# Optimization experiments

Hardware: AMD Instinct MI355X
Metric: run time of the kernel (lower is better)

## Reference

```python
import jax, jax.numpy as jnp
import numpy as np

K = 16          # neighbors (min(k, N) with N=1024 -> 16)
HID = 64        # hidden_dim
NFEAT = 64      # num_features
LN_EPS = 1e-5


def _block(h, W, b, g, beta, a):
    # Linear -> LayerNorm -> PReLU (single shared slope a, torch default)
    h = jnp.einsum('...i,oi->...o', h, W) + b
    mu = jnp.mean(h, axis=-1, keepdims=True)
    var = jnp.mean((h - mu) ** 2, axis=-1, keepdims=True)
    h = g * (h - mu) / jnp.sqrt(var + LN_EPS) + beta
    return jnp.where(h > 0, h, a * h)


def setup_inputs() -> dict:
    key = jax.random.key(0)
    ks = jax.random.split(key, 12)
    B, N, D, F, H = 16, 1024, 3, NFEAT, HID
    points = jax.random.normal(ks[0], (B, N, D), dtype=jnp.float32)
    x = jax.random.normal(ks[1], (B, N, F), dtype=jnp.float32)
    mask = jax.random.randint(ks[2], (B, N), 0, 2, dtype=jnp.int32)
    s0 = 1.0 / np.sqrt(2 * F)
    sh = 1.0 / np.sqrt(H)
    W0 = jax.random.uniform(ks[3], (H, 2 * F), jnp.float32, -s0, s0)
    b0 = jax.random.uniform(ks[4], (H,), jnp.float32, -s0, s0)
    Wh = jax.random.uniform(ks[5], (4, H, H), jnp.float32, -sh, sh)  # 3 hidden + 1 final
    bh = jax.random.uniform(ks[6], (4, H), jnp.float32, -sh, sh)
    ln_g = jnp.ones((5, H), dtype=jnp.float32)
    ln_b = jnp.zeros((5, H), dtype=jnp.float32)
    prelu_a = jnp.full((5,), 0.25, dtype=jnp.float32)
    return {"points": points, "x": x, "mask": mask, "W0": W0, "b0": b0,
            "Wh": Wh, "bh": bh, "ln_g": ln_g, "ln_b": ln_b, "prelu_a": prelu_a}


def reference(points, x, mask, W0, b0, Wh, bh, ln_g, ln_b, prelu_a):
    B, N, _ = points.shape
    F = x.shape[-1]
    # pairwise euclidean distances, invalid columns -> +inf
    delta = points[:, :, None, :] - points[:, None, :, :]          # [B,N,N,D]
    dist = jnp.sqrt(jnp.sum(delta * delta, axis=-1))               # [B,N,N]
    dist = jnp.where(mask.astype(bool)[:, None, :], dist, jnp.inf)
    # k smallest distances -> neighbor indices
    _, idx = jax.lax.top_k(-dist, K)                               # [B,N,K]
    n_tracks = jnp.sum(mask.astype(jnp.float32), axis=-1)          # [B]
    neighbors = x[jnp.arange(B)[:, None, None], idx]               # [B,N,K,F]
    xc = jnp.broadcast_to(x[:, :, None, :], (B, N, K, F))
    h = jnp.concatenate([xc, x[:, :, None, :] - neighbors], axis=-1)  # [B,N,K,2F]
    h = _block(h, W0, b0, ln_g[0], ln_b[0], prelu_a[0])
    for i in range(4):
        h = _block(h, Wh[i], bh[i], ln_g[i + 1], ln_b[i + 1], prelu_a[i + 1])
    # masked mean over neighbor slots (mask uses original n_tracks)
    nm = (jnp.arange(K)[None, None, :] < n_tracks[:, None, None]).astype(jnp.float32)  # [B,N,K]
    n_safe = jnp.where(n_tracks == 0, 1.0, n_tracks)
    aggregated = jnp.sum(h * nm[..., None], axis=-2) / n_safe[:, None, None]
    return aggregated
```

## Files before the change

### kernel.cpp

```cpp
#include <hip/hip_runtime.h>
#include <hip/hip_bf16.h>
#include <math.h>

#define N_ 1024
#define KNN_K 16
#define LN_EPS 1e-5f

typedef unsigned long long u64;
typedef unsigned int u32;
typedef __attribute__((ext_vector_type(4))) float f32x4;
typedef __attribute__((ext_vector_type(8))) short short8;
typedef __attribute__((ext_vector_type(2))) unsigned int u32x2;
typedef __attribute__((ext_vector_type(4))) unsigned int u32x4;

__device__ __forceinline__ u32 rn_hi32(float v) {
  u32 u = __float_as_uint(v);
  return (u + 0x7FFFu + ((u >> 16) & 1u)) & 0xFFFF0000u;
}
__device__ __forceinline__ u32 rn_b16(float v) {
  u32 u = __float_as_uint(v);
  return (u + 0x7FFFu + ((u >> 16) & 1u)) >> 16;
}

__global__ __launch_bounds__(256) void front_kernel(
    const float* __restrict__ Wh, u32x4* __restrict__ whi,
    u32x4* __restrict__ wlo, const int* __restrict__ mask,
    float* __restrict__ ntr, const float* __restrict__ points,
    int* __restrict__ knn, const float* __restrict__ x,
    const float* __restrict__ W0, const float* __restrict__ b0,
    float* __restrict__ p_c, float* __restrict__ p_n) {
  __shared__ float SM[8192];
  const int blk = blockIdx.x;
  const int t = threadIdx.x;

  if (blk < 8) {
    int idx = blk * 256 + t;
    int lane = idx & 63;
    int ks = (idx >> 6) & 1;
    int m = (idx >> 7) & 3;
    int li = idx >> 9;
    int o = 16 * m + (lane & 15);
    int k0 = 32 * ks + 8 * (lane >> 4);
    const float* w = Wh + li * 4096 + o * 64 + k0;
    u32x4 hi, lo;
#pragma unroll
    for (int j = 0; j < 4; j++) {
      float f0 = w[2 * j], f1 = w[2 * j + 1];
      u32 h0 = rn_hi32(f0);
      u32 h1 = rn_hi32(f1);
      float l0 = f0 - __uint_as_float(h0);
      float l1 = f1 - __uint_as_float(h1);
      hi[j] = (h0 >> 16) | h1;
      lo[j] = rn_b16(l0) | (rn_b16(l1) << 16);
    }
    int fi = ((li * 4 + m) * 2 + ks) * 64 + lane;
    whi[fi] = hi;
    wlo[fi] = lo;
  } else if (blk < 24) {
    int b = blk - 8;
    int s = 0;
    for (int e = t; e < N_; e += 256) s += mask[b * N_ + e];
    for (int off = 32; off; off >>= 1) s += __shfl_xor(s, off, 64);
    int* accI = (int*)SM;
    int wave = t >> 6, lane = t & 63;
    if (lane == 0) accI[wave] = s;
    __syncthreads();
    if (t == 0) ntr[b] = (float)(accI[0] + accI[1] + accI[2] + accI[3]);
  } else if (blk < 24 + 4096) {
#pragma clang fp contract(off)
    float* px = SM;
    float* py = SM + 1024;
    float* pz = SM + 2048;
    float* minf = SM + 3072;
    int kb = blk - 24;
    int b = kb >> 8;
    int qbase = (kb & 255) << 2;
    for (int j = t; j < N_; j += 256) {
      const float* p = points + ((size_t)(b * N_ + j)) * 3;
      px[j] = p[0];
      py[j] = p[1];
      pz[j] = p[2];
      minf[j] = mask[b * N_ + j] ? 0.0f : __builtin_inff();
    }
    __syncthreads();
    int wave = t >> 6, lane = t & 63;
    int n = qbase + wave;
    float qx = px[n], qy = py[n], qz = pz[n];
    u64 key[16];
#pragma unroll
    for (int c = 0; c < 16; c++) {
      int j = lane + (c << 6);
      float dx = qx - px[j];
      float dy = qy - py[j];
      float dz = qz - pz[j];
      float d2 = dx * dx + dy * dy + dz * dz;
      d2 = d2 + minf[j];
      key[c] = ((u64)__float_as_uint(d2) << 32) | (u32)j;
    }
    int* dst = knn + ((size_t)(b * N_ + n)) * KNN_K;
    for (int s = 0; s < 16; s++) {
      u64 m = key[0];
#pragma unroll
      for (int c = 1; c < 16; c++) m = key[c] < m ? key[c] : m;
#pragma unroll
      for (int off = 32; off; off >>= 1) {
        u64 o = __shfl_xor(m, off, 64);
        if (o < m) m = o;
      }
      if (lane == 0) dst[s] = (int)(m & 0xFFFFFFFFu);
#pragma unroll
      for (int c = 0; c < 16; c++)
        if (key[c] == m) key[c] = ~0ULL;
    }
  } else {
    float* Wc = SM;
    float* Wn = SM + 4096;
    int pb = blk - (24 + 4096);
    for (int e = t; e < 4096; e += 256) {
      int o = e & 63, i = e >> 6;
      float wa = W0[o * 128 + i];
      float wb = W0[o * 128 + 64 + i];
      Wc[i * 64 + o] = wa + wb;
      Wn[i * 64 + o] = wb;
    }
    __syncthreads();
    int wave = t >> 6, lane = t & 63;
    int pbase = pb * 64 + wave * 16;
    for (int it = 0; it < 16; it++) {
      int p = pbase + it;
      const float* xr = x + (size_t)__builtin_amdgcn_readfirstlane(p) * 64;
      float pc = b0[lane];
      float pn = 0.0f;
#pragma unroll
      for (int i = 0; i < 64; i++) {
        float xi = xr[i];
        pc = fmaf(xi, Wc[i * 64 + lane], pc);
        pn = fmaf(xi, Wn[i * 64 + lane], pn);
      }
      p_c[(size_t)p * 64 + lane] = pc;
      p_n[(size_t)p * 64 + lane] = pn;
    }
  }
}

__global__ __launch_bounds__(128) void layerA_kernel(
    const float* __restrict__ p_c, const float* __restrict__ p_n,
    const int* __restrict__ knn_, const u32x4* __restrict__ whi,
    const u32x4* __restrict__ wlo, const float* __restrict__ bh,
    const float* __restrict__ ln_g, const float* __restrict__ ln_b,
    const float* __restrict__ prelu_a, u32* __restrict__ Hout) {
  const int t = threadIdx.x;
  const int wv = t >> 6, l = t & 63;
  const int c = l & 15;
  const int g = l >> 4;
  const int pbase = blockIdx.x * 8 + wv * 4;
  const int b = pbase >> 10;

  u32x4 bhi[4][2], blo[4][2];

  {
    float h[64];
    int p0 = pbase + g;
    int j = knn_[(size_t)p0 * 16 + c];
    const float4* pc4 = reinterpret_cast<const float4*>(p_c + (size_t)p0 * 64);
    const float4* pn4 = reinterpret_cast<const float4*>(p_n + (size_t)((b << 10) + j) * 64);
#pragma unroll
    for (int q = 0; q < 16; q++) {
      float4 a = pc4[q], v = pn4[q];
      h[q * 4 + 0] = a.x - v.x;
      h[q * 4 + 1] = a.y - v.y;
      h[q * 4 + 2] = a.z - v.z;
      h[q * 4 + 3] = a.w - v.w;
    }
    float s = 0.0f, s2 = 0.0f;
#pragma unroll
    for (int o = 0; o < 64; o++) { s += h[o]; s2 += h[o] * h[o]; }
    float mu = s * (1.0f / 64.0f);
    float var = s2 * (1.0f / 64.0f) - mu * mu;
    float inv = rsqrtf(var + LN_EPS);
    float aslope = prelu_a[0];
#pragma unroll
    for (int o = 0; o < 64; o++) {
      float v = ln_g[o] * ((h[o] - mu) * inv) + ln_b[o];
      h[o] = v > 0.0f ? v : aslope * v;
    }
    u32 hpk_hi[32], hpk_lo[32];
#pragma unroll
    for (int w = 0; w < 32; w++) {
      float f0 = h[2 * w], f1 = h[2 * w + 1];
      u32 h0 = rn_hi32(f0);
      u32 h1 = rn_hi32(f1);
      float l0 = f0 - __uint_as_float(h0);
      float l1 = f1 - __uint_as_float(h1);
      hpk_hi[w] = (h0 >> 16) | h1;
      hpk_lo[w] = rn_b16(l0) | (rn_b16(l1) << 16);
    }
#pragma unroll
    for (int nt = 0; nt < 4; nt++) {
      int src = c + 16 * nt;
#pragma unroll
      for (int ks = 0; ks < 2; ks++)
#pragma unroll
        for (int gw = 0; gw < 4; gw++)
#pragma unroll
          for (int j2 = 0; j2 < 4; j2++) {
            u32 th = (u32)__shfl((int)hpk_hi[16 * ks + 4 * gw + j2], src, 64);
            u32 tl = (u32)__shfl((int)hpk_lo[16 * ks + 4 * gw + j2], src, 64);
            if (g == gw) {
              bhi[nt][ks][j2] = th;
              blo[nt][ks][j2] = tl;
            }
          }
    }
  }

  const int li = 0;
  f32x4 bias4[4];
#pragma unroll
  for (int m = 0; m < 4; m++)
    bias4[m] = *(const f32x4*)(bh + li * 64 + 16 * m + 4 * g);

  f32x4 acc[4][4];
#pragma unroll
  for (int m = 0; m < 4; m++)
#pragma unroll
    for (int nt = 0; nt < 4; nt++) acc[m][nt] = bias4[m];

#pragma unroll
  for (int ks = 0; ks < 2; ks++)
#pragma unroll
    for (int m = 0; m < 4; m++) {
      int fi = ((li * 4 + m) * 2 + ks) * 64 + l;
      short8 ah = __builtin_bit_cast(short8, whi[fi]);
      short8 al = __builtin_bit_cast(short8, wlo[fi]);
#pragma unroll
      for (int nt = 0; nt < 4; nt++) {
        short8 bh_ = __builtin_bit_cast(short8, bhi[nt][ks]);
        short8 bl_ = __builtin_bit_cast(short8, blo[nt][ks]);
        acc[m][nt] = __builtin_amdgcn_mfma_f32_16x16x32_bf16(ah, bh_, acc[m][nt], 0, 0, 0);
        acc[m][nt] = __builtin_amdgcn_mfma_f32_16x16x32_bf16(ah, bl_, acc[m][nt], 0, 0, 0);
        acc[m][nt] = __builtin_amdgcn_mfma_f32_16x16x32_bf16(al, bh_, acc[m][nt], 0, 0, 0);
      }
    }

  f32x4 g4[4], b4[4];
#pragma unroll
  for (int m = 0; m < 4; m++) {
    g4[m] = *(const f32x4*)(ln_g + (li + 1) * 64 + 16 * m + 4 * g);
    b4[m] = *(const f32x4*)(ln_b + (li + 1) * 64 + 16 * m + 4 * g);
  }
  float aslope = prelu_a[li + 1];
#pragma unroll
  for (int nt = 0; nt < 4; nt++) {
    float s = 0.0f, s2 = 0.0f;
#pragma unroll
    for (int m = 0; m < 4; m++)
#pragma unroll
      for (int v = 0; v < 4; v++) {
        float x = acc[m][nt][v];
        s += x;
        s2 = fmaf(x, x, s2);
      }
    s += __shfl_xor(s, 16, 64);
    s2 += __shfl_xor(s2, 16, 64);
    s += __shfl_xor(s, 32, 64);
    s2 += __shfl_xor(s2, 32, 64);
    float mu = s * (1.0f / 64.0f);
    float var = s2 * (1.0f / 64.0f) - mu * mu;
    float inv = rsqrtf(var + LN_EPS);
#pragma unroll
    for (int m = 0; m < 4; m++)
#pragma unroll
      for (int v = 0; v < 4; v++) {
        float x = (acc[m][nt][v] - mu) * inv;
        x = g4[m][v] * x + b4[m][v];
        acc[m][nt][v] = x > 0.0f ? x : aslope * x;
      }
  }

#pragma unroll
  for (int nt = 0; nt < 4; nt++) {
    size_t eb = ((size_t)(pbase + nt) * 16 + c) * 32;
#pragma unroll
    for (int m = 0; m < 4; m++) {
      u32x2 v;
      v[0] = rn_b16(acc[m][nt][0]) | (rn_b16(acc[m][nt][1]) << 16);
      v[1] = rn_b16(acc[m][nt][2]) | (rn_b16(acc[m][nt][3]) << 16);
      *(u32x2*)(Hout + eb + 8 * m + 2 * g) = v;
    }
  }
}

__global__ __launch_bounds__(128) void layer_kernel(
    const u32* __restrict__ Hin, u32* __restrict__ Hout,
    const u32x4* __restrict__ whi, const u32x4* __restrict__ wlo,
    const float* __restrict__ bh, const float* __restrict__ ln_g,
    const float* __restrict__ ln_b, const float* __restrict__ prelu_a,
    const float* __restrict__ ntr, float* __restrict__ out, int li, int last) {
  const int t = threadIdx.x;
  const int wv = t >> 6, l = t & 63;
  const int c = l & 15;
  const int g = l >> 4;
  const int pbase = blockIdx.x * 8 + wv * 4;
  const int b = pbase >> 10;

  u32x4 bw[4][2];
#pragma unroll
  for (int nt = 0; nt < 4; nt++) {
    size_t eb = ((size_t)(pbase + nt) * 16 + c) * 32;
#pragma unroll
    for (int ks = 0; ks < 2; ks++)
      bw[nt][ks] = *(const u32x4*)(Hin + eb + 16 * ks + 4 * g);
  }

  f32x4 bias4[4];
#pragma unroll
  for (int m = 0; m < 4; m++)
    bias4[m] = *(const f32x4*)(bh + li * 64 + 16 * m + 4 * g);

  f32x4 acc[4][4];
#pragma unroll
  for (int m = 0; m < 4; m++)
#pragma unroll
    for (int nt = 0; nt < 4; nt++) acc[m][nt] = bias4[m];

#pragma unroll
  for (int ks = 0; ks < 2; ks++)
#pragma unroll
    for (int m = 0; m < 4; m++) {
      int fi = ((li * 4 + m) * 2 + ks) * 64 + l;
      short8 ah = __builtin_bit_cast(short8, whi[fi]);
      short8 al = __builtin_bit_cast(short8, wlo[fi]);
#pragma unroll
      for (int nt = 0; nt < 4; nt++) {
        short8 bb = __builtin_bit_cast(short8, bw[nt][ks]);
        acc[m][nt] = __builtin_amdgcn_mfma_f32_16x16x32_bf16(ah, bb, acc[m][nt], 0, 0, 0);
        acc[m][nt] = __builtin_amdgcn_mfma_f32_16x16x32_bf16(al, bb, acc[m][nt], 0, 0, 0);
      }
    }

  f32x4 g4[4], b4[4];
#pragma unroll
  for (int m = 0; m < 4; m++) {
    g4[m] = *(const f32x4*)(ln_g + (li + 1) * 64 + 16 * m + 4 * g);
    b4[m] = *(const f32x4*)(ln_b + (li + 1) * 64 + 16 * m + 4 * g);
  }
  float aslope = prelu_a[li + 1];
#pragma unroll
  for (int nt = 0; nt < 4; nt++) {
    float s = 0.0f, s2 = 0.0f;
#pragma unroll
    for (int m = 0; m < 4; m++)
#pragma unroll
      for (int v = 0; v < 4; v++) {
        float x = acc[m][nt][v];
        s += x;
        s2 = fmaf(x, x, s2);
      }
    s += __shfl_xor(s, 16, 64);
    s2 += __shfl_xor(s2, 16, 64);
    s += __shfl_xor(s, 32, 64);
    s2 += __shfl_xor(s2, 32, 64);
    float mu = s * (1.0f / 64.0f);
    float var = s2 * (1.0f / 64.0f) - mu * mu;
    float inv = rsqrtf(var + LN_EPS);
#pragma unroll
    for (int m = 0; m < 4; m++)
#pragma unroll
      for (int v = 0; v < 4; v++) {
        float x = (acc[m][nt][v] - mu) * inv;
        x = g4[m][v] * x + b4[m][v];
        acc[m][nt][v] = x > 0.0f ? x : aslope * x;
      }
  }

  if (!last) {
#pragma unroll
    for (int nt = 0; nt < 4; nt++) {
      size_t eb = ((size_t)(pbase + nt) * 16 + c) * 32;
#pragma unroll
      for (int m = 0; m < 4; m++) {
        u32x2 v;
        v[0] = rn_b16(acc[m][nt][0]) | (rn_b16(acc[m][nt][1]) << 16);
        v[1] = rn_b16(acc[m][nt][2]) | (rn_b16(acc[m][nt][3]) << 16);
        *(u32x2*)(Hout + eb + 8 * m + 2 * g) = v;
      }
    }
  } else {
    float cnt = ntr[b];
    float n_safe = (cnt == 0.0f) ? 1.0f : cnt;
    float rinv = 1.0f / n_safe;
    float msk = ((float)c < cnt) ? 1.0f : 0.0f;
#pragma unroll
    for (int nt = 0; nt < 4; nt++)
#pragma unroll
      for (int m = 0; m < 4; m++) {
        f32x4 r;
#pragma unroll
        for (int v = 0; v < 4; v++) {
          float x = acc[m][nt][v] * msk;
          x += __shfl_xor(x, 1, 64);
          x += __shfl_xor(x, 2, 64);
          x += __shfl_xor(x, 4, 64);
          x += __shfl_xor(x, 8, 64);
          r[v] = x * rinv;
        }
        if (c == 0)
          *(f32x4*)(out + (size_t)(pbase + nt) * 64 + 16 * m + 4 * g) = r;
      }
  }
}

__global__ __launch_bounds__(128) void mlp_mfma3_kernel(
    const float* __restrict__ p_c, const float* __restrict__ p_n,
    const int* __restrict__ knn_, const u32x4* __restrict__ whi,
    const u32x4* __restrict__ wlo, const float* __restrict__ bh,
    const float* __restrict__ ln_g, const float* __restrict__ ln_b,
    const float* __restrict__ prelu_a, const float* __restrict__ ntr,
    float* __restrict__ out) {
  const int t = threadIdx.x;
  const int wv = t >> 6, l = t & 63;
  const int c = l & 15;
  const int g = l >> 4;
  const int pbase = blockIdx.x * 8 + wv * 4;
  const int b = pbase >> 10;

  u32x4 bhi[4][2], blo[4][2];

  {
    float h[64];
    int p0 = pbase + g;
    int j = knn_[(size_t)p0 * 16 + c];
    const float4* pc4 = reinterpret_cast<const float4*>(p_c + (size_t)p0 * 64);
    const float4* pn4 = reinterpret_cast<const float4*>(p_n + (size_t)((b << 10) + j) * 64);
#pragma unroll
    for (int q = 0; q < 16; q++) {
      float4 a = pc4[q], v = pn4[q];
      h[q * 4 + 0] = a.x - v.x;
      h[q * 4 + 1] = a.y - v.y;
      h[q * 4 + 2] = a.z - v.z;
      h[q * 4 + 3] = a.w - v.w;
    }
    float s = 0.0f, s2 = 0.0f;
#pragma unroll
    for (int o = 0; o < 64; o++) { s += h[o]; s2 += h[o] * h[o]; }
    float mu = s * (1.0f / 64.0f);
    float var = s2 * (1.0f / 64.0f) - mu * mu;
    float inv = rsqrtf(var + LN_EPS);
    float aslope = prelu_a[0];
#pragma unroll
    for (int o = 0; o < 64; o++) {
      float v = ln_g[o] * ((h[o] - mu) * inv) + ln_b[o];
      h[o] = v > 0.0f ? v : aslope * v;
    }
    u32 hpk_hi[32], hpk_lo[32];
#pragma unroll
    for (int w = 0; w < 32; w++) {
      float f0 = h[2 * w], f1 = h[2 * w + 1];
      u32 h0 = rn_hi32(f0);
      u32 h1 = rn_hi32(f1);
      float l0 = f0 - __uint_as_float(h0);
      float l1 = f1 - __uint_as_float(h1);
      hpk_hi[w] = (h0 >> 16) | h1;
      hpk_lo[w] = rn_b16(l0) | (rn_b16(l1) << 16);
    }
#pragma unroll
    for (int nt = 0; nt < 4; nt++) {
      int src = c + 16 * nt;
#pragma unroll
      for (int ks = 0; ks < 2; ks++)
#pragma unroll
        for (int gw = 0; gw < 4; gw++)
#pragma unroll
          for (int j2 = 0; j2 < 4; j2++) {
            u32 th = (u32)__shfl((int)hpk_hi[16 * ks + 4 * gw + j2], src, 64);
            u32 tl = (u32)__shfl((int)hpk_lo[16 * ks + 4 * gw + j2], src, 64);
            if (g == gw) {
              bhi[nt][ks][j2] = th;
              blo[nt][ks][j2] = tl;
            }
          }
    }
  }

  float cnt = ntr[b];

#pragma unroll 1
  for (int li = 0; li < 4; li++) {
    f32x4 bias4[4];
#pragma unroll
    for (int m = 0; m < 4; m++)
      bias4[m] = *(const f32x4*)(bh + li * 64 + 16 * m + 4 * g);

    f32x4 acc[4][4];
#pragma unroll
    for (int m = 0; m < 4; m++)
#pragma unroll
      for (int nt = 0; nt < 4; nt++) acc[m][nt] = bias4[m];

#pragma unroll
    for (int ks = 0; ks < 2; ks++)
#pragma unroll
      for (int m = 0; m < 4; m++) {
        int fi = ((li * 4 + m) * 2 + ks) * 64 + l;
        short8 ah = __builtin_bit_cast(short8, whi[fi]);
        short8 al = __builtin_bit_cast(short8, wlo[fi]);
#pragma unroll
        for (int nt = 0; nt < 4; nt++) {
          short8 bh_ = __builtin_bit_cast(short8, bhi[nt][ks]);
          short8 bl_ = __builtin_bit_cast(short8, blo[nt][ks]);
          acc[m][nt] = __builtin_amdgcn_mfma_f32_16x16x32_bf16(ah, bh_, acc[m][nt], 0, 0, 0);
          acc[m][nt] = __builtin_amdgcn_mfma_f32_16x16x32_bf16(ah, bl_, acc[m][nt], 0, 0, 0);
          acc[m][nt] = __builtin_amdgcn_mfma_f32_16x16x32_bf16(al, bh_, acc[m][nt], 0, 0, 0);
        }
      }

    f32x4 g4[4], b4[4];
#pragma unroll
    for (int m = 0; m < 4; m++) {
      g4[m] = *(const f32x4*)(ln_g + (li + 1) * 64 + 16 * m + 4 * g);
      b4[m] = *(const f32x4*)(ln_b + (li + 1) * 64 + 16 * m + 4 * g);
    }
    float aslope = prelu_a[li + 1];
#pragma unroll
    for (int nt = 0; nt < 4; nt++) {
      float s = 0.0f, s2 = 0.0f;
#pragma unroll
      for (int m = 0; m < 4; m++)
#pragma unroll
        for (int v = 0; v < 4; v++) {
          float x = acc[m][nt][v];
          s += x;
          s2 = fmaf(x, x, s2);
        }
      s += __shfl_xor(s, 16, 64);
      s2 += __shfl_xor(s2, 16, 64);
      s += __shfl_xor(s, 32, 64);
      s2 += __shfl_xor(s2, 32, 64);
      float mu = s * (1.0f / 64.0f);
      float var = s2 * (1.0f / 64.0f) - mu * mu;
      float inv = rsqrtf(var + LN_EPS);
#pragma unroll
      for (int m = 0; m < 4; m++)
#pragma unroll
        for (int v = 0; v < 4; v++) {
          float x = (acc[m][nt][v] - mu) * inv;
          x = g4[m][v] * x + b4[m][v];
          acc[m][nt][v] = x > 0.0f ? x : aslope * x;
        }
    }

    if (li < 3) {
      float h[64];
#pragma unroll
      for (int o = 0; o < 64; o++) {
        int srcl = c + 16 * ((o >> 2) & 3);
#pragma unroll
        for (int ntp = 0; ntp < 4; ntp++) {
          float tv = __shfl(acc[o >> 4][ntp][o & 3], srcl, 64);
          if (g == ntp) h[o] = tv;
        }
      }
      u32 hpk_hi[32], hpk_lo[32];
#pragma unroll
      for (int w = 0; w < 32; w++) {
        float f0 = h[2 * w], f1 = h[2 * w + 1];
        u32 h0 = rn_hi32(f0);
        u32 h1 = rn_hi32(f1);
        float l0 = f0 - __uint_as_float(h0);
        float l1 = f1 - __uint_as_float(h1);
        hpk_hi[w] = (h0 >> 16) | h1;
        hpk_lo[w] = rn_b16(l0) | (rn_b16(l1) << 16);
      }
#pragma unroll
      for (int nt = 0; nt < 4; nt++) {
        int src = c + 16 * nt;
#pragma unroll
        for (int ks = 0; ks < 2; ks++)
#pragma unroll
          for (int gw = 0; gw < 4; gw++)
#pragma unroll
            for (int j2 = 0; j2 < 4; j2++) {
              u32 th = (u32)__shfl((int)hpk_hi[16 * ks + 4 * gw + j2], src, 64);
              u32 tl = (u32)__shfl((int)hpk_lo[16 * ks + 4 * gw + j2], src, 64);
              if (g == gw) {
                bhi[nt][ks][j2] = th;
                blo[nt][ks][j2] = tl;
              }
            }
      }
    } else {
      float n_safe = (cnt == 0.0f) ? 1.0f : cnt;
      float rinv = 1.0f / n_safe;
      float msk = ((float)c < cnt) ? 1.0f : 0.0f;
#pragma unroll
      for (int nt = 0; nt < 4; nt++)
#pragma unroll
        for (int m = 0; m < 4; m++) {
          f32x4 r;
#pragma unroll
          for (int v = 0; v < 4; v++) {
            float x = acc[m][nt][v] * msk;
            x += __shfl_xor(x, 1, 64);
            x += __shfl_xor(x, 2, 64);
            x += __shfl_xor(x, 4, 64);
            x += __shfl_xor(x, 8, 64);
            r[v] = x * rinv;
          }
          if (c == 0)
            *(f32x4*)(out + (size_t)(pbase + nt) * 64 + 16 * m + 4 * g) = r;
        }
    }
  }
}

extern "C" void kernel_launch(void* const* d_in, const int* in_sizes, int n_in,
                              void* d_out, int out_size, void* d_ws, size_t ws_size,
                              hipStream_t stream) {
  const float* points  = (const float*)d_in[0];
  const float* x       = (const float*)d_in[1];
  const int*   mask    = (const int*)d_in[2];
  const float* W0      = (const float*)d_in[3];
  const float* b0      = (const float*)d_in[4];
  const float* Wh      = (const float*)d_in[5];
  const float* bh      = (const float*)d_in[6];
  const float* ln_g    = (const float*)d_in[7];
  const float* ln_b    = (const float*)d_in[8];
  const float* prelu_a = (const float*)d_in[9];
  float* out = (float*)d_out;

  char* ws = (char*)d_ws;
  int*   knn  = (int*)ws;
  float* p_c  = (float*)(ws + (1 << 20));
  float* p_n  = (float*)(ws + (1 << 20) + (4 << 20));
  u32x4* whi  = (u32x4*)(ws + (9 << 20));
  u32x4* wlo  = (u32x4*)(ws + (9 << 20) + (32 << 10));
  float* ntr  = (float*)(ws + (9 << 20) + (64 << 10));
  u32*   H0   = (u32*)(ws + ((size_t)10 << 20));
  u32*   H1   = (u32*)(ws + ((size_t)42 << 20));

  front_kernel<<<24 + 4096 + 256, 256, 0, stream>>>(
      Wh, whi, wlo, mask, ntr, points, knn, x, W0, b0, p_c, p_n);

  if (ws_size >= ((size_t)74 << 20)) {
    layerA_kernel<<<2048, 128, 0, stream>>>(p_c, p_n, knn, whi, wlo, bh,
                                            ln_g, ln_b, prelu_a, H0);
    layer_kernel<<<2048, 128, 0, stream>>>(H0, H1, whi, wlo, bh, ln_g, ln_b,
                                           prelu_a, ntr, out, 1, 0);
    layer_kernel<<<2048, 128, 0, stream>>>(H1, H0, whi, wlo, bh, ln_g, ln_b,
                                           prelu_a, ntr, out, 2, 0);
    layer_kernel<<<2048, 128, 0, stream>>>(H0, H1, whi, wlo, bh, ln_g, ln_b,
                                           prelu_a, ntr, out, 3, 1);
  } else {
    mlp_mfma3_kernel<<<2048, 128, 0, stream>>>(p_c, p_n, knn, whi, wlo, bh,
                                               ln_g, ln_b, prelu_a, ntr, out);
  }
}
```

Before: 199.0 us.

## Halve front kernel LDS and use tree reduction for kNN minimum

```diff
diff --git a/kernel.cpp b/kernel.cpp
--- a/kernel.cpp
+++ b/kernel.cpp
@@ -21,6 +21,7 @@
   u32 u = __float_as_uint(v);
   return (u + 0x7FFFu + ((u >> 16) & 1u)) >> 16;
 }
+__device__ __forceinline__ u64 umin64(u64 a, u64 b) { return a < b ? a : b; }
 
 __global__ __launch_bounds__(256) void front_kernel(
     const float* __restrict__ Wh, u32x4* __restrict__ whi,
@@ -29,7 +30,7 @@
     int* __restrict__ knn, const float* __restrict__ x,
     const float* __restrict__ W0, const float* __restrict__ b0,
     float* __restrict__ p_c, float* __restrict__ p_n) {
-  __shared__ float SM[8192];
+  __shared__ float SM[4096];
   const int blk = blockIdx.x;
   const int t = threadIdx.x;
 
@@ -99,9 +100,19 @@
     }
     int* dst = knn + ((size_t)(b * N_ + n)) * KNN_K;
     for (int s = 0; s < 16; s++) {
-      u64 m = key[0];
-#pragma unroll
-      for (int c = 1; c < 16; c++) m = key[c] < m ? key[c] : m;
+      u64 a0 = umin64(key[0], key[1]);
+      u64 a1 = umin64(key[2], key[3]);
+      u64 a2 = umin64(key[4], key[5]);
+      u64 a3 = umin64(key[6], key[7]);
+      u64 a4 = umin64(key[8], key[9]);
+      u64 a5 = umin64(key[10], key[11]);
+      u64 a6 = umin64(key[12], key[13]);
+      u64 a7 = umin64(key[14], key[15]);
+      u64 b0_ = umin64(a0, a1);
+      u64 b1_ = umin64(a2, a3);
+      u64 b2_ = umin64(a4, a5);
+      u64 b3_ = umin64(a6, a7);
+      u64 m = umin64(umin64(b0_, b1_), umin64(b2_, b3_));
 #pragma unroll
       for (int off = 32; off; off >>= 1) {
         u64 o = __shfl_xor(m, off, 64);
@@ -113,31 +124,35 @@
         if (key[c] == m) key[c] = ~0ULL;
     }
   } else {
-    float* Wc = SM;
-    float* Wn = SM + 4096;
+    float* W = SM;
     int pb = blk - (24 + 4096);
+    int wave = t >> 6, lane = t & 63;
+    int pbase = pb * 64 + wave * 16;
     for (int e = t; e < 4096; e += 256) {
       int o = e & 63, i = e >> 6;
-      float wa = W0[o * 128 + i];
-      float wb = W0[o * 128 + 64 + i];
-      Wc[i * 64 + o] = wa + wb;
-      Wn[i * 64 + o] = wb;
+      W[i * 64 + o] = W0[o * 128 + i] + W0[o * 128 + 64 + i];
     }
     __syncthreads();
-    int wave = t >> 6, lane = t & 63;
-    int pbase = pb * 64 + wave * 16;
     for (int it = 0; it < 16; it++) {
       int p = pbase + it;
       const float* xr = x + (size_t)__builtin_amdgcn_readfirstlane(p) * 64;
       float pc = b0[lane];
+#pragma unroll
+      for (int i = 0; i < 64; i++) pc = fmaf(xr[i], W[i * 64 + lane], pc);
+      p_c[(size_t)p * 64 + lane] = pc;
+    }
+    __syncthreads();
+    for (int e = t; e < 4096; e += 256) {
+      int o = e & 63, i = e >> 6;
+      W[i * 64 + o] = W0[o * 128 + 64 + i];
+    }
+    __syncthreads();
+    for (int it = 0; it < 16; it++) {
+      int p = pbase + it;
+      const float* xr = x + (size_t)__builtin_amdgcn_readfirstlane(p) * 64;
       float pn = 0.0f;
 #pragma unroll
-      for (int i = 0; i < 64; i++) {
-        float xi = xr[i];
-        pc = fmaf(xi, Wc[i * 64 + lane], pc);
-        pn = fmaf(xi, Wn[i * 64 + lane], pn);
-      }
-      p_c[(size_t)p * 64 + lane] = pc;
+      for (int i = 0; i < 64; i++) pn = fmaf(xr[i], W[i * 64 + lane], pn);
       p_n[(size_t)p * 64 + lane] = pn;
     }
   }
```

Measured after the change: 188.6 us, median of 2. 5.2% less time.
